# Kernel optimization log

Hardware: AMD Instinct MI355X
Metric: run time of the kernel (lower is better)

## Reference

```python
import jax, jax.numpy as jnp
import numpy as np
from jax import lax

B, C, H, W = 16, 3, 512, 512


def _nms(heat):
    # 3x3 max-pool, stride 1, SAME padding; keep only local peaks
    hmax = lax.reduce_window(heat, -jnp.inf, lax.max,
                             (1, 1, 3, 3), (1, 1, 1, 1), 'SAME')
    return heat * (hmax == heat).astype(heat.dtype)


def _topk(scores, K):
    b, c, h, w = scores.shape
    # per-class topk over the spatial plane
    topk_scores, topk_inds = lax.top_k(scores.reshape(b, c, h * w), K)  # [b,c,K]
    topk_row = (topk_inds // w).astype(scores.dtype)
    topk_col = (topk_inds % w).astype(scores.dtype)
    # global topk across (class, K)
    topk_score, topk_ind = lax.top_k(topk_scores.reshape(b, c * K), K)  # [b,K]
    topk_clses = topk_ind // K
    gath = lambda x: jnp.take_along_axis(x.reshape(b, c * K), topk_ind, axis=1)
    return topk_score, gath(topk_inds), topk_clses, gath(topk_row), gath(topk_col)


def _transpose_and_gather_feat(feat, inds):
    b, ch, h, w = feat.shape
    f = feat.transpose(0, 2, 3, 1).reshape(b, h * w, ch)  # [b,HW,ch]
    return jnp.take_along_axis(f, inds[:, :, None], axis=1)  # [b,K,ch]


def _decode(hm, cen_offset, direction, z_coor, dim, K):
    b = hm.shape[0]
    hm = _nms(hm)
    scores, inds, clses, row, col = _topk(hm, K)
    off = _transpose_and_gather_feat(cen_offset, inds)           # [b,K,2]
    col = col[:, :, None] + off[:, :, 0:1]
    row = row[:, :, None] + off[:, :, 1:2]
    direction = _transpose_and_gather_feat(direction, inds)      # [b,K,2]
    z_coor = _transpose_and_gather_feat(z_coor, inds)            # [b,K,1]
    dim = _transpose_and_gather_feat(dim, inds)                  # [b,K,3]
    clses = clses[:, :, None].astype(hm.dtype)
    scores = scores[:, :, None]
    return jnp.concatenate([scores, col, row, z_coor, dim, direction, clses], axis=2)


def setup_inputs() -> dict:
    key = jax.random.key(0)
    k1, k2, k3, k4, k5 = jax.random.split(key, 5)
    return {
        'hm_cen': jax.random.normal(k1, (B, C, H, W), jnp.float32),
        'cen_offset': jax.random.normal(k2, (B, 2, H, W), jnp.float32),
        'direction': jax.random.normal(k3, (B, 2, H, W), jnp.float32),
        'z_coor': jax.random.normal(k4, (B, 1, H, W), jnp.float32),
        'dim': jax.random.normal(k5, (B, 3, H, W), jnp.float32),
        'K': 500,
    }


def reference(hm_cen, cen_offset, direction, z_coor, dim, K):
    # postprocessing_v2 applies sigmoid to the class heatmap before decode
    heat = jax.nn.sigmoid(hm_cen)
    return _decode(heat, cen_offset, direction, z_coor, dim, K)  # [B,K,10]
```

## Files before the change

### kernel.cpp

```cpp
#include <hip/hip_runtime.h>
#include <math.h>
#include <float.h>

#define Hd 512
#define Wd 512
#define HWp (Hd*Wd)
#define Bn 16
#define Cn 3
#define NMAP (Bn*Cn)
#define KTOP 500
#define P_SPLIT 16
#define BAND 32
#define ROWS_W 4

__device__ __forceinline__ uint32_t flipbits(float v){
  uint32_t u = __float_as_uint(v);
  return u ^ (0x80000000u | (uint32_t)(-(int32_t)(u>>31)));
}
__device__ __forceinline__ float unflipbits(uint32_t f){
  uint32_t u = f ^ ((f>>31)? 0x80000000u : 0xFFFFFFFFu);
  return __uint_as_float(u);
}

__device__ __forceinline__ void nms_row(
    const float4 p0, const float4 p1, const float4 c0, const float4 c1,
    const float4 n0, const float4 n1, const int lane,
    uint32_t& pk, float* cv)
{
  float vm0 = fmaxf(fmaxf(p0.x,c0.x),n0.x);
  float vm1 = fmaxf(fmaxf(p0.y,c0.y),n0.y);
  float vm2 = fmaxf(fmaxf(p0.z,c0.z),n0.z);
  float vm3 = fmaxf(fmaxf(p0.w,c0.w),n0.w);
  float vm4 = fmaxf(fmaxf(p1.x,c1.x),n1.x);
  float vm5 = fmaxf(fmaxf(p1.y,c1.y),n1.y);
  float vm6 = fmaxf(fmaxf(p1.z,c1.z),n1.z);
  float vm7 = fmaxf(fmaxf(p1.w,c1.w),n1.w);
  float vmL = __shfl_up(vm7, 1);   if (lane == 0)  vmL = -INFINITY;
  float vmR = __shfl_down(vm0, 1); if (lane == 63) vmR = -INFINITY;

  float m0 = fmaxf(vmL, fmaxf(vm0, vm1));
  float m1 = fmaxf(vm0, fmaxf(vm1, vm2));
  float m2 = fmaxf(vm1, fmaxf(vm2, vm3));
  float m3 = fmaxf(vm2, fmaxf(vm3, vm4));
  float m4 = fmaxf(vm3, fmaxf(vm4, vm5));
  float m5 = fmaxf(vm4, fmaxf(vm5, vm6));
  float m6 = fmaxf(vm5, fmaxf(vm6, vm7));
  float m7 = fmaxf(vm6, fmaxf(vm7, vmR));

  pk = 0;
  if (c0.x >= m0) pk |= 1u;
  if (c0.y >= m1) pk |= 2u;
  if (c0.z >= m2) pk |= 4u;
  if (c0.w >= m3) pk |= 8u;
  if (c1.x >= m4) pk |= 16u;
  if (c1.y >= m5) pk |= 32u;
  if (c1.z >= m6) pk |= 64u;
  if (c1.w >= m7) pk |= 128u;
  cv[0]=c0.x; cv[1]=c0.y; cv[2]=c0.z; cv[3]=c0.w;
  cv[4]=c1.x; cv[5]=c1.y; cv[6]=c1.z; cv[7]=c1.w;
}

__device__ __forceinline__ void append_row(
    const uint32_t pk, const float* cv, const uint32_t ibase,
    uint32_t* __restrict__ ctr, uint64_t* __restrict__ dst, const uint32_t cap,
    uint32_t* __restrict__ hist, const int lane)
{
  const uint32_t np = (uint32_t)__popc(pk);
  uint32_t incl = np;
  #pragma unroll
  for (int d = 1; d < 64; d <<= 1) { uint32_t u = __shfl_up(incl, d); if (lane >= d) incl += u; }
  const uint32_t tot = __shfl(incl, 63);
  if (!tot) return;
  uint32_t b0 = 0;
  if (lane == 0) b0 = atomicAdd(ctr, tot);
  b0 = __shfl(b0, 0);
  uint32_t pos = b0 + incl - np;
  #pragma unroll
  for (int i = 0; i < 8; ++i) {
    if ((pk >> i) & 1u) {
      const uint32_t fb = flipbits(cv[i]);
      if (pos < cap) dst[pos] = ((uint64_t)fb << 32) | (uint32_t)(~(ibase + (uint32_t)i));
      atomicAdd(&hist[fb >> 22], 1u);
      ++pos;
    }
  }
}

__device__ __forceinline__ void findT512(
    const uint32_t* hist, const uint32_t target, const int tid, const int lane,
    const int wid, uint32_t* wtot, uint32_t* res)
{
  const uint32_t s = hist[2*tid] + hist[2*tid+1];
  uint32_t v = s;
  #pragma unroll
  for (int d = 1; d < 64; d <<= 1) { uint32_t u = __shfl_down(v, d); if (lane + d < 64) v += u; }
  if (lane == 0) wtot[wid] = v;
  __syncthreads();
  uint32_t above = 0;
  for (int ww = wid + 1; ww < 8; ++ww) above += wtot[ww];
  const uint32_t gsuf = v + above;
  if (gsuf >= target && (gsuf - s) < target) {
    uint32_t cum = gsuf - s;
    for (int b = 2*tid + 1; b >= 2*tid; --b) {
      cum += hist[b];
      if (cum >= target) { res[0]=(uint32_t)b; res[1]=target-(cum-hist[b]); res[2]=cum; break; }
    }
  }
  __syncthreads();
}

__device__ __forceinline__ uint64_t cexch(uint64_t mine, uint64_t part, bool wantMax) {
  uint64_t mx = mine > part ? mine : part;
  uint64_t mn = mine > part ? part : mine;
  return wantMax ? mx : mn;
}

__device__ void bitonic512_reg(uint64_t& e0, uint64_t* sbuf, int tid, int lane)
{
  for (int k = 2; k <= 512; k <<= 1) {
    for (int j = k >> 1; j > 0; j >>= 1) {
      const bool up = ((tid & k) == 0);
      if (j >= 64) {
        __syncthreads();
        sbuf[tid] = e0;
        __syncthreads();
        uint64_t q = sbuf[tid ^ j];
        e0 = cexch(e0, q, up == ((tid & j) == 0));
      } else {
        uint64_t q = __shfl_xor((unsigned long long)e0, j);
        e0 = cexch(e0, q, up == ((lane & j) == 0));
      }
    }
  }
  __syncthreads();
  sbuf[tid] = e0;
  __syncthreads();
}

__device__ void sort1024_lds(uint64_t* a, int tid)
{
  for (int k = 2; k <= 1024; k <<= 1) {
    for (int j = k >> 1; j > 0; j >>= 1) {
      __syncthreads();
      const int lj = 31 - __clz(j);
      const int i  = ((tid >> lj) << (lj + 1)) | (tid & (j - 1));
      const int ixj = i | j;
      const uint64_t x = a[i], y = a[ixj];
      const bool up = ((i & k) == 0);
      const bool sw = up ? (x < y) : (x > y);
      if (sw) { a[i] = y; a[ixj] = x; }
    }
  }
  __syncthreads();
}

__global__ __launch_bounds__(512) void k_fused(
    const float* __restrict__ hm, uint64_t* __restrict__ l500)
{
  __shared__ uint64_t sbuf[2048];
  __shared__ uint64_t csel[1024];
  __shared__ uint32_t hist[1024];
  __shared__ uint32_t wtot[8];
  __shared__ uint32_t res[4];
  __shared__ uint32_t cnt1, cnt2;

  const int m = blockIdx.x >> 4, p = blockIdx.x & (P_SPLIT - 1);
  const int tid = threadIdx.x, lane = tid & 63, w = tid >> 6;
  const uint64_t lt = (1ull << lane) - 1ull;
  const float* map = hm + (size_t)m * HWp;
  const int y0 = p * BAND + w * ROWS_W;
  const int xb = lane * 8;

  for (int i = tid; i < 1024; i += 512) hist[i] = 0;
  if (tid == 0) { cnt1 = 0; cnt2 = 0; }
  __syncthreads();

  const float4 NEG4 = make_float4(-INFINITY,-INFINITY,-INFINITY,-INFINITY);
  float4 ra[6], rb[6];
  #pragma unroll
  for (int r = 0; r < 6; ++r) {
    const int yy = y0 - 1 + r;
    if (yy >= 0 && yy < Hd) {
      const float* rp = map + (size_t)yy * Wd + xb;
      ra[r] = *(const float4*)rp; rb[r] = *(const float4*)(rp + 4);
    } else { ra[r] = NEG4; rb[r] = NEG4; }
  }

  #pragma unroll
  for (int r = 0; r < 4; ++r) {
    uint32_t pk; float cv[8];
    nms_row(ra[r], rb[r], ra[r+1], rb[r+1], ra[r+2], rb[r+2], lane, pk, cv);
    append_row(pk, cv, (uint32_t)((y0 + r) * Wd + xb), &cnt1, sbuf, 2048u, hist, lane);
  }
  __syncthreads();
  const uint32_t n = cnt1;
  const uint32_t nc = (n < 2048u) ? n : 2048u;

  uint32_t thresh20 = 0;
  if (n > 512) {
    findT512(hist, KTOP, tid, lane, w, wtot, res);
    const uint32_t T1 = res[0], krem = res[1];
    for (int i = tid; i < 1024; i += 512) hist[i] = 0;
    __syncthreads();
    #pragma unroll
    for (int s = 0; s < 4; ++s) {
      const uint32_t i = (uint32_t)tid + s * 512u;
      if (i < nc) {
        const uint32_t f = (uint32_t)(sbuf[i] >> 32);
        if ((f >> 22) == T1) atomicAdd(&hist[(f >> 12) & 1023u], 1u);
      }
    }
    __syncthreads();
    findT512(hist, krem, tid, lane, w, wtot, res);
    thresh20 = (T1 << 10) | res[0];
  }

  #pragma unroll
  for (int s = 0; s < 4; ++s) {
    const uint32_t i = (uint32_t)tid + s * 512u;
    const uint64_t kk = sbuf[i];
    const bool keep = (i < nc) && ((uint32_t)(kk >> 44) >= thresh20);
    const unsigned long long mask = __ballot(keep);
    if (mask) {
      uint32_t b = 0;
      if (lane == 0) b = atomicAdd(&cnt2, (uint32_t)__popcll(mask));
      b = __shfl(b, 0);
      if (keep) {
        const uint32_t pp = b + (uint32_t)__popcll(mask & lt);
        if (pp < 1024u) csel[pp] = kk;
      }
    }
  }
  __syncthreads();
  uint32_t M = cnt2; if (M > 1024u) M = 1024u;

  if (M <= 512u) {
    uint64_t e0 = (tid < (int)M) ? csel[tid] : 0ull;
    bitonic512_reg(e0, csel, tid, lane);
  } else {
    for (int i = (int)M + tid; i < 1024; i += 512) csel[i] = 0ull;
    sort1024_lds(csel, tid);
  }

  l500[(size_t)blockIdx.x * 512 + tid] = csel[tid];
}

__global__ __launch_bounds__(1024) void k_merge(
    const uint64_t* __restrict__ l500,
    float* __restrict__ s1_scores, uint32_t* __restrict__ s1_inds)
{
  __shared__ uint64_t ld[P_SPLIT * 512];
  const int m = blockIdx.x >> 3, h = blockIdx.x & 7;
  const int tid = threadIdx.x;
  const uint64_t* src = l500 + (size_t)m * (P_SPLIT * 512);
  for (int i = tid; i < P_SPLIT * 512; i += 1024) ld[i] = src[i];
  __syncthreads();

  const int i = h * 1024 + tid;
  const uint64_t kk = ld[i];
  const int r = i & 511, L = i >> 9;
  if (kk != 0ull && r < KTOP) {
    uint32_t pos[P_SPLIT - 1];
    #pragma unroll
    for (int d = 0; d < P_SPLIT - 1; ++d) pos[d] = 0;
    #pragma unroll
    for (int s = 512; s >= 1; s >>= 1) {
      #pragma unroll
      for (int d = 0; d < P_SPLIT - 1; ++d) {
        const uint64_t* lst = ld + (((L + 1 + d) & (P_SPLIT - 1)) << 9);
        const uint32_t idx = pos[d] + (uint32_t)s - 1u;
        const uint64_t v = (idx < 512u) ? lst[idx] : 0ull;
        if (v > kk) pos[d] += (uint32_t)s;
      }
    }
    uint32_t rank = (uint32_t)r;
    #pragma unroll
    for (int d = 0; d < P_SPLIT - 1; ++d) rank += pos[d];
    if (rank < KTOP) {
      const float v = unflipbits((uint32_t)(kk >> 32));
      s1_scores[m * 512 + rank] = 1.0f / (1.0f + expf(-v));
      s1_inds [m * 512 + rank] = ~(uint32_t)kk;
    }
  }
}

__global__ __launch_bounds__(512) void k_final(
    const float* __restrict__ s1_scores, const uint32_t* __restrict__ s1_inds,
    const float* __restrict__ cen_offset, const float* __restrict__ direction,
    const float* __restrict__ z_coor, const float* __restrict__ dimf,
    float* __restrict__ out)
{
  __shared__ float ssc[Cn][KTOP];
  const int b = blockIdx.x / Cn, c = blockIdx.x % Cn;
  const int tid = threadIdx.x;

  for (int i = tid; i < Cn * KTOP; i += 512) {
    int cc = i / KTOP, r = i - cc * KTOP;
    ssc[cc][r] = s1_scores[(b * Cn + cc) * 512 + r];
  }
  __syncthreads();

  if (tid < KTOP) {
    const int r = tid;
    const int i = c * KTOP + r;
    const uint64_t mykey = ((uint64_t)flipbits(ssc[c][r]) << 32) | (uint32_t)(~(uint32_t)i);
    int rank = r;
    #pragma unroll
    for (int cd = 1; cd < Cn; ++cd) {
      const int cc = (c + cd) % Cn;
      int lo = 0, hi = KTOP;
      while (lo < hi) {
        int mid = (lo + hi) >> 1;
        uint64_t k2 = ((uint64_t)flipbits(ssc[cc][mid]) << 32)
                    | (uint32_t)(~(uint32_t)(cc * KTOP + mid));
        if (k2 > mykey) lo = mid + 1; else hi = mid;
      }
      rank += lo;
    }
    if (rank < KTOP) {
      const float* co = cen_offset + (size_t)b * 2 * HWp;
      const float* di = direction  + (size_t)b * 2 * HWp;
      const float* zc = z_coor     + (size_t)b * HWp;
      const float* dm = dimf       + (size_t)b * 3 * HWp;
      const int bcx = b * Cn + c;
      const uint32_t ind = s1_inds[bcx * 512 + r];
      float o[10];
      o[0] = ssc[c][r];
      o[1] = (float)(ind & (Wd - 1)) + co[ind];
      o[2] = (float)(ind >> 9) + co[HWp + ind];
      o[3] = zc[ind];
      o[4] = dm[ind];
      o[5] = dm[HWp + ind];
      o[6] = dm[2 * HWp + ind];
      o[7] = di[ind];
      o[8] = di[HWp + ind];
      o[9] = (float)c;
      float* op = out + ((size_t)b * KTOP + rank) * 10;
      #pragma unroll
      for (int q = 0; q < 10; ++q) op[q] = o[q];
    }
  }
}

extern "C" void kernel_launch(void* const* d_in, const int* in_sizes, int n_in,
                              void* d_out, int out_size, void* d_ws, size_t ws_size,
                              hipStream_t stream)
{
  const float* hm         = (const float*)d_in[0];
  const float* cen_offset = (const float*)d_in[1];
  const float* direction  = (const float*)d_in[2];
  const float* z_coor     = (const float*)d_in[3];
  const float* dimf       = (const float*)d_in[4];
  float* out = (float*)d_out;

  char* ws = (char*)d_ws;
  uint64_t* l500  = (uint64_t*)ws;
  size_t o1       = (size_t)NMAP * P_SPLIT * 512 * 8;
  float*    s1_sc = (float*)(ws + o1);
  uint32_t* s1_id = (uint32_t*)(ws + o1 + (size_t)NMAP * 512 * 4);

  k_fused<<<NMAP * P_SPLIT, 512, 0, stream>>>(hm, l500);
  k_merge<<<NMAP * 8, 1024, 0, stream>>>(l500, s1_sc, s1_id);
  k_final<<<Bn * Cn, 512, 0, stream>>>(s1_sc, s1_id, cen_offset, direction, z_coor, dimf, out);
}
```

Baseline: 58.22 us.

## Halve spatial split per map and reuse candidate buffer for selection

```diff
diff --git a/kernel.cpp b/kernel.cpp
--- a/kernel.cpp
+++ b/kernel.cpp
@@ -9,9 +9,9 @@
 #define Cn 3
 #define NMAP (Bn*Cn)
 #define KTOP 500
-#define P_SPLIT 16
-#define BAND 32
-#define ROWS_W 4
+#define P_SPLIT 8
+#define BAND 64
+#define SCAP 4096
 
 __device__ __forceinline__ uint32_t flipbits(float v){
   uint32_t u = __float_as_uint(v);
@@ -157,18 +157,16 @@
 __global__ __launch_bounds__(512) void k_fused(
     const float* __restrict__ hm, uint64_t* __restrict__ l500)
 {
-  __shared__ uint64_t sbuf[2048];
-  __shared__ uint64_t csel[1024];
+  __shared__ uint64_t sbuf[SCAP];
   __shared__ uint32_t hist[1024];
   __shared__ uint32_t wtot[8];
   __shared__ uint32_t res[4];
   __shared__ uint32_t cnt1, cnt2;
 
-  const int m = blockIdx.x >> 4, p = blockIdx.x & (P_SPLIT - 1);
+  const int m = blockIdx.x >> 3, p = blockIdx.x & (P_SPLIT - 1);
   const int tid = threadIdx.x, lane = tid & 63, w = tid >> 6;
   const uint64_t lt = (1ull << lane) - 1ull;
   const float* map = hm + (size_t)m * HWp;
-  const int y0 = p * BAND + w * ROWS_W;
   const int xb = lane * 8;
 
   for (int i = tid; i < 1024; i += 512) hist[i] = 0;
@@ -176,25 +174,28 @@
   __syncthreads();
 
   const float4 NEG4 = make_float4(-INFINITY,-INFINITY,-INFINITY,-INFINITY);
-  float4 ra[6], rb[6];
-  #pragma unroll
-  for (int r = 0; r < 6; ++r) {
-    const int yy = y0 - 1 + r;
-    if (yy >= 0 && yy < Hd) {
-      const float* rp = map + (size_t)yy * Wd + xb;
-      ra[r] = *(const float4*)rp; rb[r] = *(const float4*)(rp + 4);
-    } else { ra[r] = NEG4; rb[r] = NEG4; }
-  }
-
-  #pragma unroll
-  for (int r = 0; r < 4; ++r) {
-    uint32_t pk; float cv[8];
-    nms_row(ra[r], rb[r], ra[r+1], rb[r+1], ra[r+2], rb[r+2], lane, pk, cv);
-    append_row(pk, cv, (uint32_t)((y0 + r) * Wd + xb), &cnt1, sbuf, 2048u, hist, lane);
+  #pragma unroll
+  for (int sub = 0; sub < 2; ++sub) {
+    const int y0 = p * BAND + w * 8 + sub * 4;
+    float4 ra[6], rb[6];
+    #pragma unroll
+    for (int r = 0; r < 6; ++r) {
+      const int yy = y0 - 1 + r;
+      if (yy >= 0 && yy < Hd) {
+        const float* rp = map + (size_t)yy * Wd + xb;
+        ra[r] = *(const float4*)rp; rb[r] = *(const float4*)(rp + 4);
+      } else { ra[r] = NEG4; rb[r] = NEG4; }
+    }
+    #pragma unroll
+    for (int r = 0; r < 4; ++r) {
+      uint32_t pk; float cv[8];
+      nms_row(ra[r], rb[r], ra[r+1], rb[r+1], ra[r+2], rb[r+2], lane, pk, cv);
+      append_row(pk, cv, (uint32_t)((y0 + r) * Wd + xb), &cnt1, sbuf, (uint32_t)SCAP, hist, lane);
+    }
   }
   __syncthreads();
   const uint32_t n = cnt1;
-  const uint32_t nc = (n < 2048u) ? n : 2048u;
+  const uint32_t nc = (n < (uint32_t)SCAP) ? n : (uint32_t)SCAP;
 
   uint32_t thresh20 = 0;
   if (n > 512) {
@@ -203,7 +204,7 @@
     for (int i = tid; i < 1024; i += 512) hist[i] = 0;
     __syncthreads();
     #pragma unroll
-    for (int s = 0; s < 4; ++s) {
+    for (int s = 0; s < SCAP/512; ++s) {
       const uint32_t i = (uint32_t)tid + s * 512u;
       if (i < nc) {
         const uint32_t f = (uint32_t)(sbuf[i] >> 32);
@@ -215,34 +216,50 @@
     thresh20 = (T1 << 10) | res[0];
   }
 
-  #pragma unroll
-  for (int s = 0; s < 4; ++s) {
-    const uint32_t i = (uint32_t)tid + s * 512u;
-    const uint64_t kk = sbuf[i];
-    const bool keep = (i < nc) && ((uint32_t)(kk >> 44) >= thresh20);
-    const unsigned long long mask = __ballot(keep);
-    if (mask) {
-      uint32_t b = 0;
-      if (lane == 0) b = atomicAdd(&cnt2, (uint32_t)__popcll(mask));
-      b = __shfl(b, 0);
-      if (keep) {
-        const uint32_t pp = b + (uint32_t)__popcll(mask & lt);
-        if (pp < 1024u) csel[pp] = kk;
-      }
-    }
-  }
+  uint64_t sk0,sk1,sk2,sk3,sk4,sk5,sk6,sk7;
+  bool kp0,kp1,kp2,kp3,kp4,kp5,kp6,kp7;
+  {
+    const uint32_t i0=(uint32_t)tid, i1=i0+512u, i2=i0+1024u, i3=i0+1536u,
+                   i4=i0+2048u, i5=i0+2560u, i6=i0+3072u, i7=i0+3584u;
+    sk0=sbuf[i0]; sk1=sbuf[i1]; sk2=sbuf[i2]; sk3=sbuf[i3];
+    sk4=sbuf[i4]; sk5=sbuf[i5]; sk6=sbuf[i6]; sk7=sbuf[i7];
+    kp0=(i0<nc)&&((uint32_t)(sk0>>44)>=thresh20);
+    kp1=(i1<nc)&&((uint32_t)(sk1>>44)>=thresh20);
+    kp2=(i2<nc)&&((uint32_t)(sk2>>44)>=thresh20);
+    kp3=(i3<nc)&&((uint32_t)(sk3>>44)>=thresh20);
+    kp4=(i4<nc)&&((uint32_t)(sk4>>44)>=thresh20);
+    kp5=(i5<nc)&&((uint32_t)(sk5>>44)>=thresh20);
+    kp6=(i6<nc)&&((uint32_t)(sk6>>44)>=thresh20);
+    kp7=(i7<nc)&&((uint32_t)(sk7>>44)>=thresh20);
+  }
+  __syncthreads();
+  #define APPEND1(SK, KP) {                                              \
+    const unsigned long long mask = __ballot(KP);                        \
+    if (mask) {                                                          \
+      uint32_t b = 0;                                                    \
+      if (lane == 0) b = atomicAdd(&cnt2, (uint32_t)__popcll(mask));     \
+      b = __shfl(b, 0);                                                  \
+      if (KP) {                                                          \
+        const uint32_t pp = b + (uint32_t)__popcll(mask & lt);           \
+        if (pp < 1024u) sbuf[pp] = SK;                                   \
+      }                                                                  \
+    }                                                                    \
+  }
+  APPEND1(sk0,kp0) APPEND1(sk1,kp1) APPEND1(sk2,kp2) APPEND1(sk3,kp3)
+  APPEND1(sk4,kp4) APPEND1(sk5,kp5) APPEND1(sk6,kp6) APPEND1(sk7,kp7)
+  #undef APPEND1
   __syncthreads();
   uint32_t M = cnt2; if (M > 1024u) M = 1024u;
 
   if (M <= 512u) {
-    uint64_t e0 = (tid < (int)M) ? csel[tid] : 0ull;
-    bitonic512_reg(e0, csel, tid, lane);
+    uint64_t e0 = (tid < (int)M) ? sbuf[tid] : 0ull;
+    bitonic512_reg(e0, sbuf, tid, lane);
   } else {
-    for (int i = (int)M + tid; i < 1024; i += 512) csel[i] = 0ull;
-    sort1024_lds(csel, tid);
-  }
-
-  l500[(size_t)blockIdx.x * 512 + tid] = csel[tid];
+    for (int i = (int)M + tid; i < 1024; i += 512) sbuf[i] = 0ull;
+    sort1024_lds(sbuf, tid);
+  }
+
+  l500[(size_t)blockIdx.x * 512 + tid] = sbuf[tid];
 }
 
 __global__ __launch_bounds__(1024) void k_merge(
@@ -250,36 +267,39 @@
     float* __restrict__ s1_scores, uint32_t* __restrict__ s1_inds)
 {
   __shared__ uint64_t ld[P_SPLIT * 512];
-  const int m = blockIdx.x >> 3, h = blockIdx.x & 7;
+  const int m = blockIdx.x >> 1, h = blockIdx.x & 1;
   const int tid = threadIdx.x;
   const uint64_t* src = l500 + (size_t)m * (P_SPLIT * 512);
   for (int i = tid; i < P_SPLIT * 512; i += 1024) ld[i] = src[i];
   __syncthreads();
 
-  const int i = h * 1024 + tid;
-  const uint64_t kk = ld[i];
-  const int r = i & 511, L = i >> 9;
-  if (kk != 0ull && r < KTOP) {
-    uint32_t pos[P_SPLIT - 1];
-    #pragma unroll
-    for (int d = 0; d < P_SPLIT - 1; ++d) pos[d] = 0;
-    #pragma unroll
-    for (int s = 512; s >= 1; s >>= 1) {
+  #pragma unroll
+  for (int e = 0; e < 2; ++e) {
+    const int i = h * 2048 + e * 1024 + tid;
+    const uint64_t kk = ld[i];
+    const int r = i & 511, L = i >> 9;
+    if (kk != 0ull && r < KTOP) {
+      uint32_t pos[P_SPLIT - 1];
       #pragma unroll
-      for (int d = 0; d < P_SPLIT - 1; ++d) {
-        const uint64_t* lst = ld + (((L + 1 + d) & (P_SPLIT - 1)) << 9);
-        const uint32_t idx = pos[d] + (uint32_t)s - 1u;
-        const uint64_t v = (idx < 512u) ? lst[idx] : 0ull;
-        if (v > kk) pos[d] += (uint32_t)s;
-      }
-    }
-    uint32_t rank = (uint32_t)r;
-    #pragma unroll
-    for (int d = 0; d < P_SPLIT - 1; ++d) rank += pos[d];
-    if (rank < KTOP) {
-      const float v = unflipbits((uint32_t)(kk >> 32));
-      s1_scores[m * 512 + rank] = 1.0f / (1.0f + expf(-v));
-      s1_inds [m * 512 + rank] = ~(uint32_t)kk;
+      for (int d = 0; d < P_SPLIT - 1; ++d) pos[d] = 0;
+      #pragma unroll
+      for (int s = 512; s >= 1; s >>= 1) {
+        #pragma unroll
+        for (int d = 0; d < P_SPLIT - 1; ++d) {
+          const uint64_t* lst = ld + (((L + 1 + d) & (P_SPLIT - 1)) << 9);
+          const uint32_t idx = pos[d] + (uint32_t)s - 1u;
+          const uint64_t v = (idx < 512u) ? lst[idx] : 0ull;
+          if (v > kk) pos[d] += (uint32_t)s;
+        }
+      }
+      uint32_t rank = (uint32_t)r;
+      #pragma unroll
+      for (int d = 0; d < P_SPLIT - 1; ++d) rank += pos[d];
+      if (rank < KTOP) {
+        const float v = unflipbits((uint32_t)(kk >> 32));
+        s1_scores[m * 512 + rank] = 1.0f / (1.0f + expf(-v));
+        s1_inds [m * 512 + rank] = ~(uint32_t)kk;
+      }
     }
   }
 }
@@ -360,6 +380,6 @@
   uint32_t* s1_id = (uint32_t*)(ws + o1 + (size_t)NMAP * 512 * 4);
 
   k_fused<<<NMAP * P_SPLIT, 512, 0, stream>>>(hm, l500);
-  k_merge<<<NMAP * 8, 1024, 0, stream>>>(l500, s1_sc, s1_id);
+  k_merge<<<NMAP * 2, 1024, 0, stream>>>(l500, s1_sc, s1_id);
   k_final<<<Bn * Cn, 512, 0, stream>>>(s1_sc, s1_id, cen_offset, direction, z_coor, dimf, out);
 }
```

Measured after the change: 51.43 us. 1.13x faster.

## Replace per-band top-k and merge with NMS dump plus single radix-select

Applied to the files above, without the earlier changes.

```diff
diff --git a/kernel.cpp b/kernel.cpp
--- a/kernel.cpp
+++ b/kernel.cpp
@@ -9,9 +9,9 @@
 #define Cn 3
 #define NMAP (Bn*Cn)
 #define KTOP 500
-#define P_SPLIT 16
+#define PBANDS 16
 #define BAND 32
-#define ROWS_W 4
+#define CAPB 4096
 
 __device__ __forceinline__ uint32_t flipbits(float v){
   uint32_t u = __float_as_uint(v);
@@ -60,119 +60,20 @@
   cv[4]=c1.x; cv[5]=c1.y; cv[6]=c1.z; cv[7]=c1.w;
 }
 
-__device__ __forceinline__ void append_row(
-    const uint32_t pk, const float* cv, const uint32_t ibase,
-    uint32_t* __restrict__ ctr, uint64_t* __restrict__ dst, const uint32_t cap,
-    uint32_t* __restrict__ hist, const int lane)
-{
-  const uint32_t np = (uint32_t)__popc(pk);
-  uint32_t incl = np;
-  #pragma unroll
-  for (int d = 1; d < 64; d <<= 1) { uint32_t u = __shfl_up(incl, d); if (lane >= d) incl += u; }
-  const uint32_t tot = __shfl(incl, 63);
-  if (!tot) return;
-  uint32_t b0 = 0;
-  if (lane == 0) b0 = atomicAdd(ctr, tot);
-  b0 = __shfl(b0, 0);
-  uint32_t pos = b0 + incl - np;
-  #pragma unroll
-  for (int i = 0; i < 8; ++i) {
-    if ((pk >> i) & 1u) {
-      const uint32_t fb = flipbits(cv[i]);
-      if (pos < cap) dst[pos] = ((uint64_t)fb << 32) | (uint32_t)(~(ibase + (uint32_t)i));
-      atomicAdd(&hist[fb >> 22], 1u);
-      ++pos;
-    }
-  }
-}
-
-__device__ __forceinline__ void findT512(
-    const uint32_t* hist, const uint32_t target, const int tid, const int lane,
-    const int wid, uint32_t* wtot, uint32_t* res)
-{
-  const uint32_t s = hist[2*tid] + hist[2*tid+1];
-  uint32_t v = s;
-  #pragma unroll
-  for (int d = 1; d < 64; d <<= 1) { uint32_t u = __shfl_down(v, d); if (lane + d < 64) v += u; }
-  if (lane == 0) wtot[wid] = v;
-  __syncthreads();
-  uint32_t above = 0;
-  for (int ww = wid + 1; ww < 8; ++ww) above += wtot[ww];
-  const uint32_t gsuf = v + above;
-  if (gsuf >= target && (gsuf - s) < target) {
-    uint32_t cum = gsuf - s;
-    for (int b = 2*tid + 1; b >= 2*tid; --b) {
-      cum += hist[b];
-      if (cum >= target) { res[0]=(uint32_t)b; res[1]=target-(cum-hist[b]); res[2]=cum; break; }
-    }
-  }
-  __syncthreads();
-}
-
-__device__ __forceinline__ uint64_t cexch(uint64_t mine, uint64_t part, bool wantMax) {
-  uint64_t mx = mine > part ? mine : part;
-  uint64_t mn = mine > part ? part : mine;
-  return wantMax ? mx : mn;
-}
-
-__device__ void bitonic512_reg(uint64_t& e0, uint64_t* sbuf, int tid, int lane)
-{
-  for (int k = 2; k <= 512; k <<= 1) {
-    for (int j = k >> 1; j > 0; j >>= 1) {
-      const bool up = ((tid & k) == 0);
-      if (j >= 64) {
-        __syncthreads();
-        sbuf[tid] = e0;
-        __syncthreads();
-        uint64_t q = sbuf[tid ^ j];
-        e0 = cexch(e0, q, up == ((tid & j) == 0));
-      } else {
-        uint64_t q = __shfl_xor((unsigned long long)e0, j);
-        e0 = cexch(e0, q, up == ((lane & j) == 0));
-      }
-    }
-  }
-  __syncthreads();
-  sbuf[tid] = e0;
-  __syncthreads();
-}
-
-__device__ void sort1024_lds(uint64_t* a, int tid)
-{
-  for (int k = 2; k <= 1024; k <<= 1) {
-    for (int j = k >> 1; j > 0; j >>= 1) {
-      __syncthreads();
-      const int lj = 31 - __clz(j);
-      const int i  = ((tid >> lj) << (lj + 1)) | (tid & (j - 1));
-      const int ixj = i | j;
-      const uint64_t x = a[i], y = a[ixj];
-      const bool up = ((i & k) == 0);
-      const bool sw = up ? (x < y) : (x > y);
-      if (sw) { a[i] = y; a[ixj] = x; }
-    }
-  }
-  __syncthreads();
-}
-
-__global__ __launch_bounds__(512) void k_fused(
-    const float* __restrict__ hm, uint64_t* __restrict__ l500)
-{
-  __shared__ uint64_t sbuf[2048];
-  __shared__ uint64_t csel[1024];
-  __shared__ uint32_t hist[1024];
-  __shared__ uint32_t wtot[8];
-  __shared__ uint32_t res[4];
-  __shared__ uint32_t cnt1, cnt2;
-
-  const int m = blockIdx.x >> 4, p = blockIdx.x & (P_SPLIT - 1);
+__global__ __launch_bounds__(512) void k_nms(
+    const float* __restrict__ hm, uint64_t* __restrict__ seg_all,
+    uint32_t* __restrict__ cnt)
+{
+  __shared__ uint32_t ctr;
+  const int bid = blockIdx.x;
+  const int m = bid >> 4, p = bid & (PBANDS - 1);
   const int tid = threadIdx.x, lane = tid & 63, w = tid >> 6;
-  const uint64_t lt = (1ull << lane) - 1ull;
   const float* map = hm + (size_t)m * HWp;
-  const int y0 = p * BAND + w * ROWS_W;
+  uint64_t* dst = seg_all + (size_t)bid * CAPB;
+  const int y0 = p * BAND + w * 4;
   const int xb = lane * 8;
 
-  for (int i = tid; i < 1024; i += 512) hist[i] = 0;
-  if (tid == 0) { cnt1 = 0; cnt2 = 0; }
+  if (tid == 0) ctr = 0;
   __syncthreads();
 
   const float4 NEG4 = make_float4(-INFINITY,-INFINITY,-INFINITY,-INFINITY);
@@ -190,97 +91,153 @@
   for (int r = 0; r < 4; ++r) {
     uint32_t pk; float cv[8];
     nms_row(ra[r], rb[r], ra[r+1], rb[r+1], ra[r+2], rb[r+2], lane, pk, cv);
-    append_row(pk, cv, (uint32_t)((y0 + r) * Wd + xb), &cnt1, sbuf, 2048u, hist, lane);
-  }
-  __syncthreads();
-  const uint32_t n = cnt1;
-  const uint32_t nc = (n < 2048u) ? n : 2048u;
-
-  uint32_t thresh20 = 0;
-  if (n > 512) {
-    findT512(hist, KTOP, tid, lane, w, wtot, res);
-    const uint32_t T1 = res[0], krem = res[1];
-    for (int i = tid; i < 1024; i += 512) hist[i] = 0;
+    const uint32_t np = (uint32_t)__popc(pk);
+    uint32_t incl = np;
+    #pragma unroll
+    for (int d = 1; d < 64; d <<= 1) { uint32_t u = __shfl_up(incl, d); if (lane >= d) incl += u; }
+    const uint32_t tot = __shfl(incl, 63);
+    if (!tot) continue;
+    uint32_t b0 = 0;
+    if (lane == 0) b0 = atomicAdd(&ctr, tot);
+    b0 = __shfl(b0, 0);
+    uint32_t pos = b0 + incl - np;
+    const uint32_t ib = (uint32_t)((y0 + r) * Wd + xb);
+    #pragma unroll
+    for (int i = 0; i < 8; ++i) {
+      if ((pk >> i) & 1u) {
+        if (pos < (uint32_t)CAPB)
+          dst[pos] = ((uint64_t)flipbits(cv[i]) << 32) | (uint32_t)(~(ib + (uint32_t)i));
+        ++pos;
+      }
+    }
+  }
+  __syncthreads();
+  if (tid == 0) cnt[bid] = (ctr < (uint32_t)CAPB) ? ctr : (uint32_t)CAPB;
+}
+
+__device__ __forceinline__ void findT4096(
+    const uint32_t* hist, const uint32_t target, const int tid, const int lane,
+    const int wid, uint32_t* wtot, uint32_t* res)
+{
+  const uint32_t s = hist[4*tid] + hist[4*tid+1] + hist[4*tid+2] + hist[4*tid+3];
+  uint32_t v = s;
+  #pragma unroll
+  for (int d = 1; d < 64; d <<= 1) { uint32_t u = __shfl_down(v, d); if (lane + d < 64) v += u; }
+  if (lane == 0) wtot[wid] = v;
+  __syncthreads();
+  uint32_t above = 0;
+  for (int ww = wid + 1; ww < 16; ++ww) above += wtot[ww];
+  const uint32_t gsuf = v + above;
+  if (gsuf >= target && (gsuf - s) < target) {
+    uint32_t cum = gsuf - s;
+    for (int b = 4*tid + 3; b >= 4*tid; --b) {
+      cum += hist[b];
+      if (cum >= target) { res[0]=(uint32_t)b; res[1]=target-(cum-hist[b]); res[2]=cum; break; }
+    }
+  }
+  __syncthreads();
+}
+
+__global__ __launch_bounds__(1024) void k_select(
+    const uint64_t* __restrict__ seg_all, const uint32_t* __restrict__ cnt,
+    float* __restrict__ s1_scores, uint32_t* __restrict__ s1_inds)
+{
+  __shared__ uint32_t hist[4096];
+  __shared__ uint64_t csel[1024];
+  __shared__ uint32_t wtot[16];
+  __shared__ uint32_t res[4];
+
+  const int m = blockIdx.x;
+  const int tid = threadIdx.x, lane = tid & 63, wid = tid >> 6;
+  const uint64_t lt = (1ull << lane) - 1ull;
+
+  for (int i = tid; i < 4096; i += 1024) hist[i] = 0;
+  if (tid == 0) res[3] = 0;
+  __syncthreads();
+
+  const uint64_t* sg = seg_all + (size_t)(m * PBANDS + wid) * CAPB;
+  const uint32_t sn = min(cnt[m * PBANDS + wid], (uint32_t)CAPB);
+
+  for (uint32_t base = 0; base < sn; base += 256u) {
+    const uint32_t i0 = base + (uint32_t)lane, i1 = i0 + 64u, i2 = i0 + 128u, i3 = i0 + 192u;
+    uint64_t k0 = 0, k1 = 0, k2 = 0, k3 = 0;
+    if (i0 < sn) k0 = sg[i0];
+    if (i1 < sn) k1 = sg[i1];
+    if (i2 < sn) k2 = sg[i2];
+    if (i3 < sn) k3 = sg[i3];
+    if (i0 < sn) atomicAdd(&hist[(uint32_t)(k0 >> 52)], 1u);
+    if (i1 < sn) atomicAdd(&hist[(uint32_t)(k1 >> 52)], 1u);
+    if (i2 < sn) atomicAdd(&hist[(uint32_t)(k2 >> 52)], 1u);
+    if (i3 < sn) atomicAdd(&hist[(uint32_t)(k3 >> 52)], 1u);
+  }
+  __syncthreads();
+
+  findT4096(hist, KTOP, tid, lane, wid, wtot, res);
+  const uint32_t T1 = res[0], krem = res[1], M0 = res[2];
+  __syncthreads();
+
+  uint32_t shift = 20, thr = T1;
+  if (M0 > 1024u) {
+    for (int i = tid; i < 4096; i += 1024) hist[i] = 0;
     __syncthreads();
-    #pragma unroll
-    for (int s = 0; s < 4; ++s) {
-      const uint32_t i = (uint32_t)tid + s * 512u;
-      if (i < nc) {
-        const uint32_t f = (uint32_t)(sbuf[i] >> 32);
-        if ((f >> 22) == T1) atomicAdd(&hist[(f >> 12) & 1023u], 1u);
-      }
+    for (uint32_t i = (uint32_t)lane; i < sn; i += 64u) {
+      const uint32_t f = (uint32_t)(sg[i] >> 32);
+      if ((f >> 20) == T1) atomicAdd(&hist[(f >> 8) & 4095u], 1u);
     }
     __syncthreads();
-    findT512(hist, krem, tid, lane, w, wtot, res);
-    thresh20 = (T1 << 10) | res[0];
-  }
-
-  #pragma unroll
-  for (int s = 0; s < 4; ++s) {
-    const uint32_t i = (uint32_t)tid + s * 512u;
-    const uint64_t kk = sbuf[i];
-    const bool keep = (i < nc) && ((uint32_t)(kk >> 44) >= thresh20);
-    const unsigned long long mask = __ballot(keep);
-    if (mask) {
-      uint32_t b = 0;
-      if (lane == 0) b = atomicAdd(&cnt2, (uint32_t)__popcll(mask));
-      b = __shfl(b, 0);
-      if (keep) {
-        const uint32_t pp = b + (uint32_t)__popcll(mask & lt);
-        if (pp < 1024u) csel[pp] = kk;
-      }
-    }
-  }
-  __syncthreads();
-  uint32_t M = cnt2; if (M > 1024u) M = 1024u;
-
-  if (M <= 512u) {
-    uint64_t e0 = (tid < (int)M) ? csel[tid] : 0ull;
-    bitonic512_reg(e0, csel, tid, lane);
-  } else {
-    for (int i = (int)M + tid; i < 1024; i += 512) csel[i] = 0ull;
-    sort1024_lds(csel, tid);
-  }
-
-  l500[(size_t)blockIdx.x * 512 + tid] = csel[tid];
-}
-
-__global__ __launch_bounds__(1024) void k_merge(
-    const uint64_t* __restrict__ l500,
-    float* __restrict__ s1_scores, uint32_t* __restrict__ s1_inds)
-{
-  __shared__ uint64_t ld[P_SPLIT * 512];
-  const int m = blockIdx.x >> 3, h = blockIdx.x & 7;
-  const int tid = threadIdx.x;
-  const uint64_t* src = l500 + (size_t)m * (P_SPLIT * 512);
-  for (int i = tid; i < P_SPLIT * 512; i += 1024) ld[i] = src[i];
-  __syncthreads();
-
-  const int i = h * 1024 + tid;
-  const uint64_t kk = ld[i];
-  const int r = i & 511, L = i >> 9;
-  if (kk != 0ull && r < KTOP) {
-    uint32_t pos[P_SPLIT - 1];
-    #pragma unroll
-    for (int d = 0; d < P_SPLIT - 1; ++d) pos[d] = 0;
-    #pragma unroll
-    for (int s = 512; s >= 1; s >>= 1) {
-      #pragma unroll
-      for (int d = 0; d < P_SPLIT - 1; ++d) {
-        const uint64_t* lst = ld + (((L + 1 + d) & (P_SPLIT - 1)) << 9);
-        const uint32_t idx = pos[d] + (uint32_t)s - 1u;
-        const uint64_t v = (idx < 512u) ? lst[idx] : 0ull;
-        if (v > kk) pos[d] += (uint32_t)s;
-      }
-    }
-    uint32_t rank = (uint32_t)r;
-    #pragma unroll
-    for (int d = 0; d < P_SPLIT - 1; ++d) rank += pos[d];
-    if (rank < KTOP) {
-      const float v = unflipbits((uint32_t)(kk >> 32));
-      s1_scores[m * 512 + rank] = 1.0f / (1.0f + expf(-v));
-      s1_inds [m * 512 + rank] = ~(uint32_t)kk;
-    }
+    findT4096(hist, krem, tid, lane, wid, wtot, res);
+    shift = 8; thr = (T1 << 12) | res[0];
+    __syncthreads();
+  }
+
+  for (uint32_t base = 0; base < sn; base += 256u) {
+    const uint32_t i0 = base + (uint32_t)lane, i1 = i0 + 64u, i2 = i0 + 128u, i3 = i0 + 192u;
+    uint64_t k0 = 0, k1 = 0, k2 = 0, k3 = 0;
+    if (i0 < sn) k0 = sg[i0];
+    if (i1 < sn) k1 = sg[i1];
+    if (i2 < sn) k2 = sg[i2];
+    if (i3 < sn) k3 = sg[i3];
+    const bool p0 = (i0 < sn) && (((uint32_t)(k0 >> 32) >> shift) >= thr);
+    const bool p1 = (i1 < sn) && (((uint32_t)(k1 >> 32) >> shift) >= thr);
+    const bool p2 = (i2 < sn) && (((uint32_t)(k2 >> 32) >> shift) >= thr);
+    const bool p3 = (i3 < sn) && (((uint32_t)(k3 >> 32) >> shift) >= thr);
+    #define APP(K, P) {                                                  \
+      const unsigned long long mask = __ballot(P);                       \
+      if (mask) {                                                        \
+        uint32_t b = 0;                                                  \
+        if (lane == 0) b = atomicAdd(&res[3], (uint32_t)__popcll(mask)); \
+        b = __shfl(b, 0);                                                \
+        if (P) {                                                         \
+          const uint32_t pp = b + (uint32_t)__popcll(mask & lt);         \
+          if (pp < 1024u) csel[pp] = K;                                  \
+        }                                                                \
+      }                                                                  \
+    }
+    APP(k0, p0) APP(k1, p1) APP(k2, p2) APP(k3, p3)
+    #undef APP
+  }
+  __syncthreads();
+  uint32_t M = res[3]; if (M > 1024u) M = 1024u;
+  const uint32_t Mp = (M + 3u) & ~3u;
+  if ((uint32_t)tid >= M && (uint32_t)tid < Mp) csel[tid] = 0ull;
+  __syncthreads();
+
+  const uint64_t kk = ((uint32_t)tid < M) ? csel[tid] : 0ull;
+  uint32_t rank = 0;
+  for (uint32_t j = 0; j < Mp; j += 4u) {
+    rank += (csel[j]   > kk) ? 1u : 0u;
+    rank += (csel[j+1] > kk) ? 1u : 0u;
+    rank += (csel[j+2] > kk) ? 1u : 0u;
+    rank += (csel[j+3] > kk) ? 1u : 0u;
+  }
+  if ((uint32_t)tid < M && rank < 512u) {
+    const float v = unflipbits((uint32_t)(kk >> 32));
+    s1_scores[m * 512 + rank] = 1.0f / (1.0f + expf(-v));
+    s1_inds [m * 512 + rank] = ~(uint32_t)kk;
+  }
+  if ((uint32_t)tid >= M && tid < 512) {
+    s1_scores[m * 512 + tid] = 0.0f;
+    s1_inds [m * 512 + tid] = 0u;
   }
 }
 
@@ -354,12 +311,13 @@
   float* out = (float*)d_out;
 
   char* ws = (char*)d_ws;
-  uint64_t* l500  = (uint64_t*)ws;
-  size_t o1       = (size_t)NMAP * P_SPLIT * 512 * 8;
-  float*    s1_sc = (float*)(ws + o1);
-  uint32_t* s1_id = (uint32_t*)(ws + o1 + (size_t)NMAP * 512 * 4);
-
-  k_fused<<<NMAP * P_SPLIT, 512, 0, stream>>>(hm, l500);
-  k_merge<<<NMAP * 8, 1024, 0, stream>>>(l500, s1_sc, s1_id);
-  k_final<<<Bn * Cn, 512, 0, stream>>>(s1_sc, s1_id, cen_offset, direction, z_coor, dimf, out);
-}
+  uint32_t* cnt   = (uint32_t*)ws;
+  float*    s1_sc = (float*)(ws + 4096);
+  uint32_t* s1_id = (uint32_t*)(ws + 4096 + (size_t)NMAP * 512 * 4);
+  size_t fixed    = 4096 + (size_t)NMAP * 512 * 4 * 2;
+  uint64_t* seg   = (uint64_t*)(ws + fixed);
+
+  k_nms   <<<NMAP * PBANDS, 512, 0, stream>>>(hm, seg, cnt);
+  k_select<<<NMAP,         1024, 0, stream>>>(seg, cnt, s1_sc, s1_id);
+  k_final <<<Bn * Cn,       512, 0, stream>>>(s1_sc, s1_id, cen_offset, direction, z_coor, dimf, out);
+}
```

After: 61.61 us. 5.8% more time.
